# Optimization experiments

Measured on AMD Instinct MI355X. Metric: run time of the kernel, lower is better.

## Reference

```python
import jax, jax.numpy as jnp
import numpy as np
from jax import lax

DIM = 128
HEADS = 8
HEAD_DIM = DIM // HEADS
SR = 2
B, H, W = 2, 80, 80
SCALE = HEAD_DIM ** (-0.5)
BN_EPS = 1e-5


def _conv1x1(x, w, b):
    # x: (B,C,H,W), w: (O,C), b: (O,)
    return jnp.einsum('bchw,oc->bohw', x, w) + b[None, :, None, None]


def setup_inputs() -> dict:
    key = jax.random.key(0)
    ks = jax.random.split(key, 12)
    s = DIM ** -0.5
    x = jax.random.normal(ks[0], (B, DIM, H, W), dtype=jnp.float32)
    q_w = jax.random.normal(ks[1], (DIM, DIM), dtype=jnp.float32) * s
    q_b = jnp.zeros((DIM,), jnp.float32)
    k_w = jax.random.normal(ks[2], (DIM, DIM), dtype=jnp.float32) * s
    k_b = jnp.zeros((DIM,), jnp.float32)
    v_w = jax.random.normal(ks[3], (DIM, DIM), dtype=jnp.float32) * s
    v_b = jnp.zeros((DIM,), jnp.float32)
    sr_w = jax.random.normal(ks[4], (DIM, DIM, SR, SR), dtype=jnp.float32) * (s / SR)
    sr_b = jnp.zeros((DIM,), jnp.float32)
    bn_gamma = jnp.ones((DIM,), jnp.float32)
    bn_beta = jnp.zeros((DIM,), jnp.float32)
    bn_mean = jnp.zeros((DIM,), jnp.float32)
    bn_var = jnp.ones((DIM,), jnp.float32)
    proj_w = jax.random.normal(ks[5], (DIM, DIM), dtype=jnp.float32) * s
    proj_b = jnp.zeros((DIM,), jnp.float32)
    return dict(x=x, q_w=q_w, q_b=q_b, k_w=k_w, k_b=k_b, v_w=v_w, v_b=v_b,
                sr_w=sr_w, sr_b=sr_b, bn_gamma=bn_gamma, bn_beta=bn_beta,
                bn_mean=bn_mean, bn_var=bn_var, proj_w=proj_w, proj_b=proj_b)


def reference(x, q_w, q_b, k_w, k_b, v_w, v_b, sr_w, sr_b,
              bn_gamma, bn_beta, bn_mean, bn_var, proj_w, proj_b):
    b, c, h, w = x.shape
    n = h * w
    # q: (B,h,N,d)
    q = _conv1x1(x, q_w, q_b).reshape(b, HEADS, HEAD_DIM, n).transpose(0, 1, 3, 2)
    # spatial reduction: Conv2d(k=SR, s=SR) + BN(eval) + ReLU
    x_kv = lax.conv_general_dilated(x, sr_w, window_strides=(SR, SR),
                                    padding='VALID',
                                    dimension_numbers=('NCHW', 'OIHW', 'NCHW'))
    x_kv = x_kv + sr_b[None, :, None, None]
    inv = bn_gamma / jnp.sqrt(bn_var + BN_EPS)
    x_kv = x_kv * inv[None, :, None, None] + (bn_beta - bn_mean * inv)[None, :, None, None]
    x_kv = jax.nn.relu(x_kv)
    n_kv = x_kv.shape[2] * x_kv.shape[3]
    k = _conv1x1(x_kv, k_w, k_b).reshape(b, HEADS, HEAD_DIM, n_kv).transpose(0, 1, 3, 2)
    v = _conv1x1(x_kv, v_w, v_b).reshape(b, HEADS, HEAD_DIM, n_kv).transpose(0, 1, 3, 2)
    # explicit attention: (B,h,N,N_kv)
    attn = jnp.einsum('bhnd,bhmd->bhnm', q, k) * SCALE
    attn = jax.nn.softmax(attn, axis=-1)
    out = jnp.einsum('bhnm,bhmd->bhnd', attn, v)  # (B,h,N,d)
    # faithful to source layout: transpose(1,2) then reshape to (B,C,H,W)
    out = out.transpose(0, 2, 1, 3).reshape(b, c, h, w)
    out = _conv1x1(out, proj_w, proj_b)
    return out
```

## Files before the change

kernel.cpp:

```cpp
#include <hip/hip_runtime.h>
#include <hip/hip_bf16.h>
#include <cmath>

#define DIM 128
#define HEADS 8
#define HEAD_DIM 16
#define NBATCH 2
#define HH 80
#define WW 80
#define NQ 6400
#define NKV 1600
#define NC 50
#define BN_EPS 1e-5f
#define LOG2E 1.4426950408889634f

typedef __bf16 bf16_t;
typedef __attribute__((ext_vector_type(8))) __bf16 bf16x8;
typedef __attribute__((ext_vector_type(16))) float f32x16;

union BF8U { bf16x8 v; unsigned u[4]; };

__device__ inline unsigned packbf2(float a, float b) {
  union { __hip_bfloat162 v; unsigned u; } r;
  r.v = __float22bfloat162_rn(make_float2(a, b));
  return r.u;
}

__device__ inline unsigned short f2bf(float v) {
  unsigned u = __float_as_uint(v);
  return (unsigned short)((u + 0x7FFFu + ((u >> 16) & 1u)) >> 16);
}

__global__ __launch_bounds__(256) void prep_all(
    const float* __restrict__ x,
    const float* __restrict__ qw, const float* __restrict__ kw,
    const float* __restrict__ vw, const float* __restrict__ pw,
    const float* __restrict__ srw,
    unsigned short* __restrict__ Xb,
    unsigned short* __restrict__ Wb,
    unsigned short* __restrict__ X4b,
    unsigned short* __restrict__ Vp)
{
  __shared__ float tile[32][33];
  int t = threadIdx.x;
  int bx = blockIdx.x;
  if (bx < 1600) {
    int tx = t & 31, ty = t >> 5;
    int b = bx / 800;
    int rem = bx % 800;
    int c0 = (rem / 200) * 32, s0 = (rem % 200) * 32;
#pragma unroll
    for (int r = 0; r < 32; r += 8)
      tile[ty + r][tx] = x[((size_t)b * DIM + c0 + ty + r) * NQ + s0 + tx];
    __syncthreads();
#pragma unroll
    for (int r = 0; r < 32; r += 8)
      Xb[((size_t)b * NQ + s0 + ty + r) * DIM + c0 + tx] = f2bf(tile[tx][ty + r]);
    return;
  }
  int e = (bx - 1600) * 256 + t;
  if (e < 131072) {
    const float* src; int idx;
    if (e < 16384)      { src = qw;  idx = e; }
    else if (e < 32768) { src = kw;  idx = e - 16384; }
    else if (e < 49152) { src = vw;  idx = e - 32768; }
    else if (e < 65536) { src = pw;  idx = e - 49152; }
    else                { src = srw; idx = e - 65536; }
    Wb[e] = f2bf(src[idx]);
  }
  if (e < NBATCH * HEADS * NC * 32) {
    int cid = e >> 5;
    int pos = e & 31;
    size_t addr = (size_t)cid * 1024 + 256 + ((pos & 16) ? 512 : 0) + (pos & 15);
    Vp[addr] = 0x3F80;
  }
  int c4 = e & 511;
  int r = e >> 9;
  int b = r / 1600, m = r % 1600;
  int c = c4 >> 2, ky = (c4 >> 1) & 1, kx = c4 & 1;
  int i = m / 40, j = m % 40;
  X4b[e] = f2bf(x[((size_t)b * DIM + c) * NQ + (2 * i + ky) * WW + 2 * j + kx]);
}

__global__ __launch_bounds__(256) void mgemm_qsr(
    const bf16_t* __restrict__ Xb, const bf16_t* __restrict__ X4b,
    const bf16_t* __restrict__ Wb,
    const float* __restrict__ q_b, const float* __restrict__ sr_b,
    unsigned short* __restrict__ Qb, unsigned short* __restrict__ xkvb,
    float sl,
    const float* __restrict__ bng, const float* __restrict__ bnb,
    const float* __restrict__ bnm, const float* __restrict__ bnv)
{
  int t = threadIdx.x;
  int ln = t & 31, hf = (t >> 5) & 1, wid = t >> 6;
  int b = blockIdx.y;
  bool isq = blockIdx.x < 200;
  int s0 = isq ? blockIdx.x * 32 : (blockIdx.x - 200) * 32;
  int S  = isq ? NQ : NKV;
  int C  = isq ? 128 : 512;
  const bf16_t* X = isq ? Xb : X4b;
  const bf16_t* W = isq ? Wb : (Wb + 65536);
  int o = wid * 32 + ln;

  const bf16_t* arow = &X[((size_t)b * S + s0 + ln) * C + hf * 8];
  const bf16_t* brow = &W[(size_t)o * C + hf * 8];
  f32x16 acc = {};
#pragma unroll 8
  for (int c0 = 0; c0 < C; c0 += 16) {
    bf16x8 af = *(const bf16x8*)&arow[c0];
    bf16x8 bf = *(const bf16x8*)&brow[c0];
    acc = __builtin_amdgcn_mfma_f32_32x32x16_bf16(af, bf, acc, 0, 0, 0);
  }

  float bv, a1, b2;
  bool relu;
  if (isq) { bv = q_b[o]; a1 = sl; b2 = 0.f; relu = false; }
  else {
    bv = sr_b[o];
    float inv = bng[o] / sqrtf(bnv[o] + BN_EPS);
    a1 = inv; b2 = bnb[o] - bnm[o] * inv; relu = true;
  }
  unsigned short* ob = isq ? Qb : xkvb;
#pragma unroll
  for (int g = 0; g < 4; ++g)
#pragma unroll
    for (int j = 0; j < 4; ++j) {
      float v = (acc[4 * g + j] + bv) * a1 + b2;
      if (relu) v = fmaxf(v, 0.f);
      int s = s0 + 8 * g + 4 * hf + j;
      ob[((size_t)b * S + s) * DIM + o] = f2bf(v);
    }
}

__global__ __launch_bounds__(256) void mgemm_kv(
    const bf16_t* __restrict__ xkvb, const bf16_t* __restrict__ Wb,
    const float* __restrict__ k_b, const float* __restrict__ v_b,
    unsigned short* __restrict__ Kp, unsigned short* __restrict__ Vp)
{
  int t = threadIdx.x;
  int ln = t & 31, hf = (t >> 5) & 1, wid = t >> 6;
  int b = blockIdx.y;
  int isv = blockIdx.z;
  int s0 = blockIdx.x * 32;
  const bf16_t* W = Wb + (isv ? 32768 : 16384);
  int o = wid * 32 + ln;

  const bf16_t* arow = &xkvb[((size_t)b * NKV + s0 + ln) * DIM + hf * 8];
  const bf16_t* brow = &W[(size_t)o * DIM + hf * 8];
  f32x16 acc = {};
#pragma unroll
  for (int c0 = 0; c0 < 128; c0 += 16) {
    bf16x8 af = *(const bf16x8*)&arow[c0];
    bf16x8 bf = *(const bf16x8*)&brow[c0];
    acc = __builtin_amdgcn_mfma_f32_32x32x16_bf16(af, bf, acc, 0, 0, 0);
  }

  int hloc = o >> 4, d = o & 15;
  if (isv) {
    float bv = v_b[o];
    size_t CB = (((size_t)b * HEADS + hloc) * NC + (s0 >> 5)) * 1024;
    uint4 w0, w1;
    w0.x = packbf2(acc[0] + bv, acc[1] + bv);
    w0.y = packbf2(acc[2] + bv, acc[3] + bv);
    w0.z = packbf2(acc[4] + bv, acc[5] + bv);
    w0.w = packbf2(acc[6] + bv, acc[7] + bv);
    w1.x = packbf2(acc[8] + bv, acc[9] + bv);
    w1.y = packbf2(acc[10] + bv, acc[11] + bv);
    w1.z = packbf2(acc[12] + bv, acc[13] + bv);
    w1.w = packbf2(acc[14] + bv, acc[15] + bv);
    *(uint4*)&Vp[CB + d * 16 + hf * 8] = w0;
    *(uint4*)&Vp[CB + 512 + d * 16 + hf * 8] = w1;
  } else {
    float bv = k_b[o];
    size_t CB = (((size_t)b * HEADS + hloc) * NC + (s0 >> 5)) * 512;
#pragma unroll
    for (int g = 0; g < 4; ++g)
#pragma unroll
      for (int j = 0; j < 4; ++j) {
        int sl2 = 8 * g + 4 * hf + j;
        Kp[CB + sl2 * 16 + d] = f2bf(acc[4 * g + j] + bv);
      }
  }
}

__global__ __launch_bounds__(256) void attn_split(const bf16_t* __restrict__ Qb,
                                                  const bf16_t* __restrict__ Kp,
                                                  const bf16_t* __restrict__ Vp,
                                                  unsigned short* __restrict__ Pb,
                                                  float* __restrict__ Lsum)
{
  const int t = threadIdx.x;
  const int ln = t & 31, hf = (t >> 5) & 1, wid = t >> 6;
  const int h = blockIdx.y;
  const int b = blockIdx.z & 1, half = blockIdx.z >> 1;
  const int q0 = blockIdx.x * 128 + wid * 32;

  bf16x8 qf = *(const bf16x8*)&Qb[((size_t)b * NQ + q0 + ln) * 128 + h * 16 + hf * 8];
  const int bh = b * HEADS + h;
  const bf16_t* kc = &Kp[((size_t)bh * NC + half * 25) * 512 + ln * 16 + hf * 8];
  const bf16_t* vc = &Vp[((size_t)bh * NC + half * 25) * 1024 + ln * 16 + hf * 8];

  f32x16 acc = {};
  const f32x16 zero = {};

  bf16x8 kf = *(const bf16x8*)kc;
  bf16x8 va = *(const bf16x8*)vc;
  bf16x8 vb = *(const bf16x8*)(vc + 512);

  for (int c = 0; c < 25; ++c) {
    int cn = (c < 24) ? c + 1 : c;
    bf16x8 kf2 = *(const bf16x8*)(kc + cn * 512);
    bf16x8 va2 = *(const bf16x8*)(vc + cn * 1024);
    bf16x8 vb2 = *(const bf16x8*)(vc + cn * 1024 + 512);

    f32x16 S = __builtin_amdgcn_mfma_f32_32x32x16_bf16(kf, qf, zero, 0, 0, 0);

    BF8U f0, f1;
#pragma unroll
    for (int i = 0; i < 4; ++i) {
      f0.u[i] = packbf2(__builtin_amdgcn_exp2f(S[2 * i]),
                        __builtin_amdgcn_exp2f(S[2 * i + 1]));
      f1.u[i] = packbf2(__builtin_amdgcn_exp2f(S[8 + 2 * i]),
                        __builtin_amdgcn_exp2f(S[9 + 2 * i]));
    }

    acc = __builtin_amdgcn_mfma_f32_32x32x16_bf16(va, f0.v, acc, 0, 0, 0);
    acc = __builtin_amdgcn_mfma_f32_32x32x16_bf16(vb, f1.v, acc, 0, 0, 0);
    kf = kf2; va = va2; vb = vb2;
  }

  unsigned short* prow =
      &Pb[(((size_t)(half * 2 + b)) * NQ + q0 + ln) * 128 + h * 16 + 4 * hf];
  uint2 w0, w1;
  w0.x = packbf2(acc[0], acc[1]); w0.y = packbf2(acc[2], acc[3]);
  w1.x = packbf2(acc[4], acc[5]); w1.y = packbf2(acc[6], acc[7]);
  *(uint2*)&prow[0] = w0;
  *(uint2*)&prow[8] = w1;
  if (!hf)
    Lsum[(((size_t)(half * 2 + b)) * HEADS + h) * NQ + q0 + ln] = acc[8];
}

__global__ __launch_bounds__(256) void proj_comb(const unsigned short* __restrict__ Pb,
                                                 const float* __restrict__ Lsum,
                                                 const bf16_t* __restrict__ Wb,
                                                 const float* __restrict__ bias,
                                                 float* __restrict__ Out)
{
  __shared__ unsigned short As[32][136];
  int t = threadIdx.x;
  int b = blockIdx.y;
  int s0 = blockIdx.x * 32;

  {
    int tx = t & 31, cg = t >> 5;
#pragma unroll
    for (int it = 0; it < 16; ++it) {
      int c = cg * 16 + it;
      int f = c * NQ + s0 + tx;
      int n = f >> 7, hh = (f >> 4) & 7;
      float p0 = __uint_as_float((unsigned)Pb[(size_t)b * 819200 + f] << 16);
      float p1 = __uint_as_float((unsigned)Pb[(size_t)(2 + b) * 819200 + f] << 16);
      float L = Lsum[((size_t)b * HEADS + hh) * NQ + n] +
                Lsum[((size_t)(2 + b) * HEADS + hh) * NQ + n];
      As[tx][c] = f2bf((p0 + p1) / L);
    }
  }
  __syncthreads();

  int ln = t & 31, hf = (t >> 5) & 1, wid = t >> 6;
  int o = wid * 32 + ln;
  const bf16_t* brow = &Wb[49152 + (size_t)o * DIM + hf * 8];
  const unsigned short* arow = &As[ln][hf * 8];
  f32x16 acc = {};
#pragma unroll
  for (int c0 = 0; c0 < 128; c0 += 16) {
    bf16x8 af = *(const bf16x8*)&arow[c0];
    bf16x8 bf = *(const bf16x8*)&brow[c0];
    acc = __builtin_amdgcn_mfma_f32_32x32x16_bf16(af, bf, acc, 0, 0, 0);
  }
  float bv = bias[o];
  float* obase = &Out[((size_t)b * DIM + o) * NQ + s0 + 4 * hf];
#pragma unroll
  for (int g = 0; g < 4; ++g) {
    float4 r;
    r.x = acc[4 * g + 0] + bv; r.y = acc[4 * g + 1] + bv;
    r.z = acc[4 * g + 2] + bv; r.w = acc[4 * g + 3] + bv;
    *(float4*)&obase[8 * g] = r;
  }
}

extern "C" void kernel_launch(void* const* d_in, const int* in_sizes, int n_in,
                              void* d_out, int out_size, void* d_ws, size_t ws_size,
                              hipStream_t stream)
{
  const float* x    = (const float*)d_in[0];
  const float* q_w  = (const float*)d_in[1];
  const float* q_b  = (const float*)d_in[2];
  const float* k_w  = (const float*)d_in[3];
  const float* k_b  = (const float*)d_in[4];
  const float* v_w  = (const float*)d_in[5];
  const float* v_b  = (const float*)d_in[6];
  const float* sr_w = (const float*)d_in[7];
  const float* sr_b = (const float*)d_in[8];
  const float* bng  = (const float*)d_in[9];
  const float* bnb  = (const float*)d_in[10];
  const float* bnm  = (const float*)d_in[11];
  const float* bnv  = (const float*)d_in[12];
  const float* p_w  = (const float*)d_in[13];
  const float* p_b  = (const float*)d_in[14];
  float* out = (float*)d_out;

  float* ws = (float*)d_ws;
  bf16_t* Xb   = (bf16_t*)(ws);
  bf16_t* X4b  = (bf16_t*)(ws + 819200);
  bf16_t* xkvb = (bf16_t*)(ws + 1638400);
  bf16_t* Pb   = (bf16_t*)(ws);
  bf16_t* Qb   = (bf16_t*)(ws + 1843200);
  bf16_t* Kp   = (bf16_t*)(ws + 2662400);
  bf16_t* Vp   = (bf16_t*)(ws + 2867200);
  float*  Lsum = ws + 3276800;
  bf16_t* Wb   = (bf16_t*)(ws + 3481600);

  const float sl = 0.25f * LOG2E;

  prep_all<<<dim3(8000), dim3(256), 0, stream>>>(
      x, q_w, k_w, v_w, p_w, sr_w,
      (unsigned short*)Xb, (unsigned short*)Wb,
      (unsigned short*)X4b, (unsigned short*)Vp);

  mgemm_qsr<<<dim3(250, NBATCH), dim3(256), 0, stream>>>(
      Xb, X4b, Wb, q_b, sr_b, (unsigned short*)Qb, (unsigned short*)xkvb,
      sl, bng, bnb, bnm, bnv);

  mgemm_kv<<<dim3(NKV / 32, NBATCH, 2), dim3(256), 0, stream>>>(
      xkvb, Wb, k_b, v_b, (unsigned short*)Kp, (unsigned short*)Vp);

  attn_split<<<dim3(NQ / 128, HEADS, 4), dim3(256), 0, stream>>>(
      Qb, Kp, Vp, (unsigned short*)Pb, Lsum);

  proj_comb<<<dim3(200, NBATCH), dim3(256), 0, stream>>>(
      (const unsigned short*)Pb, Lsum, Wb, p_b, out);
}
```

Before: 161.5 us.

## Fuse input prep into GEMMs, generalize attention KV split count

Removes the separate prep kernel. The Q and spatial-reduction GEMMs now read fp32 x directly, gathering the strided or 2x2 patch elements and converting to bf16 in registers. Weights are converted from fp32 on the fly in every GEMM, and the V ones-column padding moves into the V GEMM. Attention gets a configurable KV split count (4 when the workspace allows) with a simpler non-prefetching loop and launch bounds for higher occupancy, and the projection kernel reduces across all splits. This trades one launch and its intermediate buffers for uncoalesced strided global reads in the Q/SR GEMM and more partial-sum traffic.

```diff
diff --git a/kernel.cpp b/kernel.cpp
--- a/kernel.cpp
+++ b/kernel.cpp
@@ -4,10 +4,7 @@
 
 #define DIM 128
 #define HEADS 8
-#define HEAD_DIM 16
 #define NBATCH 2
-#define HH 80
-#define WW 80
 #define NQ 6400
 #define NKV 1600
 #define NC 50
@@ -31,110 +28,89 @@
   return (unsigned short)((u + 0x7FFFu + ((u >> 16) & 1u)) >> 16);
 }
 
-__global__ __launch_bounds__(256) void prep_all(
+__device__ inline bf16x8 ldw8(const float* __restrict__ p) {
+  float4 w0 = *(const float4*)p;
+  float4 w1 = *(const float4*)(p + 4);
+  BF8U r;
+  r.u[0] = packbf2(w0.x, w0.y);
+  r.u[1] = packbf2(w0.z, w0.w);
+  r.u[2] = packbf2(w1.x, w1.y);
+  r.u[3] = packbf2(w1.z, w1.w);
+  return r.v;
+}
+
+__global__ __launch_bounds__(256) void mgemm_qsr(
     const float* __restrict__ x,
-    const float* __restrict__ qw, const float* __restrict__ kw,
-    const float* __restrict__ vw, const float* __restrict__ pw,
-    const float* __restrict__ srw,
-    unsigned short* __restrict__ Xb,
-    unsigned short* __restrict__ Wb,
-    unsigned short* __restrict__ X4b,
-    unsigned short* __restrict__ Vp)
-{
-  __shared__ float tile[32][33];
-  int t = threadIdx.x;
-  int bx = blockIdx.x;
-  if (bx < 1600) {
-    int tx = t & 31, ty = t >> 5;
-    int b = bx / 800;
-    int rem = bx % 800;
-    int c0 = (rem / 200) * 32, s0 = (rem % 200) * 32;
-#pragma unroll
-    for (int r = 0; r < 32; r += 8)
-      tile[ty + r][tx] = x[((size_t)b * DIM + c0 + ty + r) * NQ + s0 + tx];
-    __syncthreads();
-#pragma unroll
-    for (int r = 0; r < 32; r += 8)
-      Xb[((size_t)b * NQ + s0 + ty + r) * DIM + c0 + tx] = f2bf(tile[tx][ty + r]);
-    return;
-  }
-  int e = (bx - 1600) * 256 + t;
-  if (e < 131072) {
-    const float* src; int idx;
-    if (e < 16384)      { src = qw;  idx = e; }
-    else if (e < 32768) { src = kw;  idx = e - 16384; }
-    else if (e < 49152) { src = vw;  idx = e - 32768; }
-    else if (e < 65536) { src = pw;  idx = e - 49152; }
-    else                { src = srw; idx = e - 65536; }
-    Wb[e] = f2bf(src[idx]);
-  }
-  if (e < NBATCH * HEADS * NC * 32) {
-    int cid = e >> 5;
-    int pos = e & 31;
-    size_t addr = (size_t)cid * 1024 + 256 + ((pos & 16) ? 512 : 0) + (pos & 15);
-    Vp[addr] = 0x3F80;
-  }
-  int c4 = e & 511;
-  int r = e >> 9;
-  int b = r / 1600, m = r % 1600;
-  int c = c4 >> 2, ky = (c4 >> 1) & 1, kx = c4 & 1;
-  int i = m / 40, j = m % 40;
-  X4b[e] = f2bf(x[((size_t)b * DIM + c) * NQ + (2 * i + ky) * WW + 2 * j + kx]);
-}
-
-__global__ __launch_bounds__(256) void mgemm_qsr(
-    const bf16_t* __restrict__ Xb, const bf16_t* __restrict__ X4b,
-    const bf16_t* __restrict__ Wb,
-    const float* __restrict__ q_b, const float* __restrict__ sr_b,
+    const float* __restrict__ q_w, const float* __restrict__ q_b,
+    const float* __restrict__ sr_w, const float* __restrict__ sr_b,
+    const float* __restrict__ bng, const float* __restrict__ bnb,
+    const float* __restrict__ bnm, const float* __restrict__ bnv,
     unsigned short* __restrict__ Qb, unsigned short* __restrict__ xkvb,
-    float sl,
-    const float* __restrict__ bng, const float* __restrict__ bnb,
-    const float* __restrict__ bnm, const float* __restrict__ bnv)
+    float sl)
 {
   int t = threadIdx.x;
   int ln = t & 31, hf = (t >> 5) & 1, wid = t >> 6;
   int b = blockIdx.y;
-  bool isq = blockIdx.x < 200;
-  int s0 = isq ? blockIdx.x * 32 : (blockIdx.x - 200) * 32;
-  int S  = isq ? NQ : NKV;
-  int C  = isq ? 128 : 512;
-  const bf16_t* X = isq ? Xb : X4b;
-  const bf16_t* W = isq ? Wb : (Wb + 65536);
   int o = wid * 32 + ln;
-
-  const bf16_t* arow = &X[((size_t)b * S + s0 + ln) * C + hf * 8];
-  const bf16_t* brow = &W[(size_t)o * C + hf * 8];
   f32x16 acc = {};
-#pragma unroll 8
-  for (int c0 = 0; c0 < C; c0 += 16) {
-    bf16x8 af = *(const bf16x8*)&arow[c0];
-    bf16x8 bf = *(const bf16x8*)&brow[c0];
-    acc = __builtin_amdgcn_mfma_f32_32x32x16_bf16(af, bf, acc, 0, 0, 0);
-  }
-
-  float bv, a1, b2;
-  bool relu;
-  if (isq) { bv = q_b[o]; a1 = sl; b2 = 0.f; relu = false; }
-  else {
-    bv = sr_b[o];
+
+  if (blockIdx.x < 200) {
+    int s0 = blockIdx.x * 32;
+    const float* ab = x + (size_t)b * DIM * NQ + s0 + ln;
+    const float* brow = q_w + (size_t)o * 128 + hf * 8;
+#pragma unroll
+    for (int c0 = 0; c0 < 128; c0 += 16) {
+      BF8U af;
+#pragma unroll
+      for (int jj = 0; jj < 4; ++jj)
+        af.u[jj] = packbf2(ab[(size_t)(c0 + hf * 8 + 2 * jj) * NQ],
+                           ab[(size_t)(c0 + hf * 8 + 2 * jj + 1) * NQ]);
+      acc = __builtin_amdgcn_mfma_f32_32x32x16_bf16(af.v, ldw8(&brow[c0]), acc, 0, 0, 0);
+    }
+    float bv = q_b[o];
+#pragma unroll
+    for (int g = 0; g < 4; ++g)
+#pragma unroll
+      for (int j = 0; j < 4; ++j) {
+        int s = s0 + 8 * g + 4 * hf + j;
+        Qb[((size_t)b * NQ + s) * DIM + o] = f2bf((acc[4 * g + j] + bv) * sl);
+      }
+  } else {
+    int s0 = (blockIdx.x - 200) * 32;
+    int m = s0 + ln;
+    int i = m / 40, jp = m % 40;
+    const float* ab = x + (size_t)b * DIM * NQ + i * 160 + 2 * jp;
+    const float* brow = sr_w + (size_t)o * 512 + hf * 8;
+#pragma unroll 4
+    for (int c0 = 0; c0 < 512; c0 += 16) {
+      BF8U af;
+#pragma unroll
+      for (int jj = 0; jj < 4; ++jj) {
+        int ca = c0 + hf * 8 + 2 * jj, cb = ca + 1;
+        float va_ = ab[(size_t)(ca >> 2) * NQ + ((ca >> 1) & 1) * 80 + (ca & 1)];
+        float vb_ = ab[(size_t)(cb >> 2) * NQ + ((cb >> 1) & 1) * 80 + (cb & 1)];
+        af.u[jj] = packbf2(va_, vb_);
+      }
+      acc = __builtin_amdgcn_mfma_f32_32x32x16_bf16(af.v, ldw8(&brow[c0]), acc, 0, 0, 0);
+    }
+    float bv = sr_b[o];
     float inv = bng[o] / sqrtf(bnv[o] + BN_EPS);
-    a1 = inv; b2 = bnb[o] - bnm[o] * inv; relu = true;
-  }
-  unsigned short* ob = isq ? Qb : xkvb;
-#pragma unroll
-  for (int g = 0; g < 4; ++g)
-#pragma unroll
-    for (int j = 0; j < 4; ++j) {
-      float v = (acc[4 * g + j] + bv) * a1 + b2;
-      if (relu) v = fmaxf(v, 0.f);
-      int s = s0 + 8 * g + 4 * hf + j;
-      ob[((size_t)b * S + s) * DIM + o] = f2bf(v);
-    }
+    float b2 = bnb[o] - bnm[o] * inv;
+#pragma unroll
+    for (int g = 0; g < 4; ++g)
+#pragma unroll
+      for (int j = 0; j < 4; ++j) {
+        int s = s0 + 8 * g + 4 * hf + j;
+        float v = fmaxf((acc[4 * g + j] + bv) * inv + b2, 0.f);
+        xkvb[((size_t)b * NKV + s) * DIM + o] = f2bf(v);
+      }
+  }
 }
 
 __global__ __launch_bounds__(256) void mgemm_kv(
-    const bf16_t* __restrict__ xkvb, const bf16_t* __restrict__ Wb,
-    const float* __restrict__ k_b, const float* __restrict__ v_b,
+    const bf16_t* __restrict__ xkvb,
+    const float* __restrict__ k_w, const float* __restrict__ k_b,
+    const float* __restrict__ v_w, const float* __restrict__ v_b,
     unsigned short* __restrict__ Kp, unsigned short* __restrict__ Vp)
 {
   int t = threadIdx.x;
@@ -142,17 +118,16 @@
   int b = blockIdx.y;
   int isv = blockIdx.z;
   int s0 = blockIdx.x * 32;
-  const bf16_t* W = Wb + (isv ? 32768 : 16384);
+  const float* W = isv ? v_w : k_w;
   int o = wid * 32 + ln;
 
   const bf16_t* arow = &xkvb[((size_t)b * NKV + s0 + ln) * DIM + hf * 8];
-  const bf16_t* brow = &W[(size_t)o * DIM + hf * 8];
+  const float* brow = W + (size_t)o * DIM + hf * 8;
   f32x16 acc = {};
 #pragma unroll
   for (int c0 = 0; c0 < 128; c0 += 16) {
     bf16x8 af = *(const bf16x8*)&arow[c0];
-    bf16x8 bf = *(const bf16x8*)&brow[c0];
-    acc = __builtin_amdgcn_mfma_f32_32x32x16_bf16(af, bf, acc, 0, 0, 0);
+    acc = __builtin_amdgcn_mfma_f32_32x32x16_bf16(af, ldw8(&brow[c0]), acc, 0, 0, 0);
   }
 
   int hloc = o >> 4, d = o & 15;
@@ -170,6 +145,11 @@
     w1.w = packbf2(acc[14] + bv, acc[15] + bv);
     *(uint4*)&Vp[CB + d * 16 + hf * 8] = w0;
     *(uint4*)&Vp[CB + 512 + d * 16 + hf * 8] = w1;
+    {
+      int h2 = t >> 5, pos = t & 31;
+      size_t CB2 = (((size_t)b * HEADS + h2) * NC + (s0 >> 5)) * 1024;
+      Vp[CB2 + 256 + ((pos & 16) ? 512 : 0) + (pos & 15)] = 0x3F80;
+    }
   } else {
     float bv = k_b[o];
     size_t CB = (((size_t)b * HEADS + hloc) * NC + (s0 >> 5)) * 512;
@@ -183,35 +163,33 @@
   }
 }
 
-__global__ __launch_bounds__(256) void attn_split(const bf16_t* __restrict__ Qb,
-                                                  const bf16_t* __restrict__ Kp,
-                                                  const bf16_t* __restrict__ Vp,
-                                                  unsigned short* __restrict__ Pb,
-                                                  float* __restrict__ Lsum)
+__global__ __launch_bounds__(256, 8) void attn_split(
+    const bf16_t* __restrict__ Qb, const bf16_t* __restrict__ Kp,
+    const bf16_t* __restrict__ Vp, unsigned short* __restrict__ Pb,
+    float* __restrict__ Lsum, int nsplit)
 {
   const int t = threadIdx.x;
   const int ln = t & 31, hf = (t >> 5) & 1, wid = t >> 6;
   const int h = blockIdx.y;
-  const int b = blockIdx.z & 1, half = blockIdx.z >> 1;
+  const int b = blockIdx.z & 1, quarter = blockIdx.z >> 1;
   const int q0 = blockIdx.x * 128 + wid * 32;
-
-  bf16x8 qf = *(const bf16x8*)&Qb[((size_t)b * NQ + q0 + ln) * 128 + h * 16 + hf * 8];
+  const int base = NC / nsplit, rem = NC % nsplit;
+  const int kcnt = base + (quarter < rem ? 1 : 0);
+  const int kstart = quarter * base + (quarter < rem ? quarter : rem);
+  const int slice = quarter * 2 + b;
+
+  bf16x8 qf = *(const bf16x8*)&Qb[((size_t)b * NQ + q0 + ln) * DIM + h * 16 + hf * 8];
   const int bh = b * HEADS + h;
-  const bf16_t* kc = &Kp[((size_t)bh * NC + half * 25) * 512 + ln * 16 + hf * 8];
-  const bf16_t* vc = &Vp[((size_t)bh * NC + half * 25) * 1024 + ln * 16 + hf * 8];
+  const bf16_t* kc = &Kp[((size_t)bh * NC + kstart) * 512 + ln * 16 + hf * 8];
+  const bf16_t* vc = &Vp[((size_t)bh * NC + kstart) * 1024 + ln * 16 + hf * 8];
 
   f32x16 acc = {};
   const f32x16 zero = {};
 
-  bf16x8 kf = *(const bf16x8*)kc;
-  bf16x8 va = *(const bf16x8*)vc;
-  bf16x8 vb = *(const bf16x8*)(vc + 512);
-
-  for (int c = 0; c < 25; ++c) {
-    int cn = (c < 24) ? c + 1 : c;
-    bf16x8 kf2 = *(const bf16x8*)(kc + cn * 512);
-    bf16x8 va2 = *(const bf16x8*)(vc + cn * 1024);
-    bf16x8 vb2 = *(const bf16x8*)(vc + cn * 1024 + 512);
+  for (int c = 0; c < kcnt; ++c) {
+    bf16x8 kf = *(const bf16x8*)kc;
+    bf16x8 va = *(const bf16x8*)vc;
+    bf16x8 vb = *(const bf16x8*)(vc + 512);
 
     f32x16 S = __builtin_amdgcn_mfma_f32_32x32x16_bf16(kf, qf, zero, 0, 0, 0);
 
@@ -226,25 +204,24 @@
 
     acc = __builtin_amdgcn_mfma_f32_32x32x16_bf16(va, f0.v, acc, 0, 0, 0);
     acc = __builtin_amdgcn_mfma_f32_32x32x16_bf16(vb, f1.v, acc, 0, 0, 0);
-    kf = kf2; va = va2; vb = vb2;
+    kc += 512; vc += 1024;
   }
 
   unsigned short* prow =
-      &Pb[(((size_t)(half * 2 + b)) * NQ + q0 + ln) * 128 + h * 16 + 4 * hf];
+      &Pb[(size_t)slice * (NQ * DIM) + (size_t)(q0 + ln) * DIM + h * 16 + 4 * hf];
   uint2 w0, w1;
   w0.x = packbf2(acc[0], acc[1]); w0.y = packbf2(acc[2], acc[3]);
   w1.x = packbf2(acc[4], acc[5]); w1.y = packbf2(acc[6], acc[7]);
   *(uint2*)&prow[0] = w0;
   *(uint2*)&prow[8] = w1;
   if (!hf)
-    Lsum[(((size_t)(half * 2 + b)) * HEADS + h) * NQ + q0 + ln] = acc[8];
-}
-
-__global__ __launch_bounds__(256) void proj_comb(const unsigned short* __restrict__ Pb,
-                                                 const float* __restrict__ Lsum,
-                                                 const bf16_t* __restrict__ Wb,
-                                                 const float* __restrict__ bias,
-                                                 float* __restrict__ Out)
+    Lsum[(size_t)slice * (HEADS * NQ) + (size_t)h * NQ + q0 + ln] = acc[8];
+}
+
+__global__ __launch_bounds__(256) void proj_comb(
+    const unsigned short* __restrict__ Pb, const float* __restrict__ Lsum,
+    const float* __restrict__ p_w, const float* __restrict__ p_b,
+    float* __restrict__ Out, int nsplit)
 {
   __shared__ unsigned short As[32][136];
   int t = threadIdx.x;
@@ -258,27 +235,28 @@
       int c = cg * 16 + it;
       int f = c * NQ + s0 + tx;
       int n = f >> 7, hh = (f >> 4) & 7;
-      float p0 = __uint_as_float((unsigned)Pb[(size_t)b * 819200 + f] << 16);
-      float p1 = __uint_as_float((unsigned)Pb[(size_t)(2 + b) * 819200 + f] << 16);
-      float L = Lsum[((size_t)b * HEADS + hh) * NQ + n] +
-                Lsum[((size_t)(2 + b) * HEADS + hh) * NQ + n];
-      As[tx][c] = f2bf((p0 + p1) / L);
+      float ps = 0.f, L = 0.f;
+      for (int qq = 0; qq < nsplit; ++qq) {
+        int sl2 = qq * 2 + b;
+        ps += __uint_as_float((unsigned)Pb[(size_t)sl2 * (NQ * DIM) + f] << 16);
+        L += Lsum[(size_t)sl2 * (HEADS * NQ) + (size_t)hh * NQ + n];
+      }
+      As[tx][c] = f2bf(ps / L);
     }
   }
   __syncthreads();
 
   int ln = t & 31, hf = (t >> 5) & 1, wid = t >> 6;
   int o = wid * 32 + ln;
-  const bf16_t* brow = &Wb[49152 + (size_t)o * DIM + hf * 8];
+  const float* brow = p_w + (size_t)o * DIM + hf * 8;
   const unsigned short* arow = &As[ln][hf * 8];
   f32x16 acc = {};
 #pragma unroll
   for (int c0 = 0; c0 < 128; c0 += 16) {
     bf16x8 af = *(const bf16x8*)&arow[c0];
-    bf16x8 bf = *(const bf16x8*)&brow[c0];
-    acc = __builtin_amdgcn_mfma_f32_32x32x16_bf16(af, bf, acc, 0, 0, 0);
-  }
-  float bv = bias[o];
+    acc = __builtin_amdgcn_mfma_f32_32x32x16_bf16(af, ldw8(&brow[c0]), acc, 0, 0, 0);
+  }
+  float bv = p_b[o];
   float* obase = &Out[((size_t)b * DIM + o) * NQ + s0 + 4 * hf];
 #pragma unroll
   for (int g = 0; g < 4; ++g) {
@@ -310,34 +288,29 @@
   const float* p_b  = (const float*)d_in[14];
   float* out = (float*)d_out;
 
+  const int nsplit = (ws_size >= (size_t)5120000 * 4) ? 4 : 2;
+
   float* ws = (float*)d_ws;
-  bf16_t* Xb   = (bf16_t*)(ws);
-  bf16_t* X4b  = (bf16_t*)(ws + 819200);
-  bf16_t* xkvb = (bf16_t*)(ws + 1638400);
-  bf16_t* Pb   = (bf16_t*)(ws);
-  bf16_t* Qb   = (bf16_t*)(ws + 1843200);
-  bf16_t* Kp   = (bf16_t*)(ws + 2662400);
-  bf16_t* Vp   = (bf16_t*)(ws + 2867200);
-  float*  Lsum = ws + 3276800;
-  bf16_t* Wb   = (bf16_t*)(ws + 3481600);
+  bf16_t* Pb   = (bf16_t*)ws;
+  bf16_t* xkvb = (bf16_t*)ws;
+  size_t off = (size_t)nsplit * 819200;
+  bf16_t* Qb = (bf16_t*)(ws + off);   off += 819200;
+  bf16_t* Kp = (bf16_t*)(ws + off);   off += 204800;
+  bf16_t* Vp = (bf16_t*)(ws + off);   off += 409600;
+  float* Lsum = ws + off;
 
   const float sl = 0.25f * LOG2E;
 
-  prep_all<<<dim3(8000), dim3(256), 0, stream>>>(
-      x, q_w, k_w, v_w, p_w, sr_w,
-      (unsigned short*)Xb, (unsigned short*)Wb,
-      (unsigned short*)X4b, (unsigned short*)Vp);
-
   mgemm_qsr<<<dim3(250, NBATCH), dim3(256), 0, stream>>>(
-      Xb, X4b, Wb, q_b, sr_b, (unsigned short*)Qb, (unsigned short*)xkvb,
-      sl, bng, bnb, bnm, bnv);
+      x, q_w, q_b, sr_w, sr_b, bng, bnb, bnm, bnv,
+      (unsigned short*)Qb, (unsigned short*)xkvb, sl);
 
   mgemm_kv<<<dim3(NKV / 32, NBATCH, 2), dim3(256), 0, stream>>>(
-      xkvb, Wb, k_b, v_b, (unsigned short*)Kp, (unsigned short*)Vp);
-
-  attn_split<<<dim3(NQ / 128, HEADS, 4), dim3(256), 0, stream>>>(
-      Qb, Kp, Vp, (unsigned short*)Pb, Lsum);
+      xkvb, k_w, k_b, v_w, v_b, (unsigned short*)Kp, (unsigned short*)Vp);
+
+  attn_split<<<dim3(NQ / 128, HEADS, 2 * nsplit), dim3(256), 0, stream>>>(
+      Qb, Kp, Vp, (unsigned short*)Pb, Lsum, nsplit);
 
   proj_comb<<<dim3(200, NBATCH), dim3(256), 0, stream>>>(
-      (const unsigned short*)Pb, Lsum, Wb, p_b, out);
-}
+      (const unsigned short*)Pb, Lsum, p_w, p_b, out, nsplit);
+}
```

After: 168.6 us. 1.04x slower.

## Generalize attention KV split to configurable count, use four splits when workspace allows

Applied to the files above, without the earlier changes.

The attention kernel now splits the KV chunks across a runtime-chosen number of partitions (four if the workspace is large enough, else two), raising the block count from 800 to 1600 for more parallelism on the GPU. The projection kernel sums the partial outputs and softmax denominators over all splits. The Pb buffer moves to its own workspace region instead of aliasing Xb, and the software prefetch of the next K/V chunk is removed in favor of plain in-loop loads with an occupancy hint. The cost is more partial-result traffic and extra reduction work in the combine step.

```diff
diff --git a/kernel.cpp b/kernel.cpp
--- a/kernel.cpp
+++ b/kernel.cpp
@@ -4,10 +4,7 @@
 
 #define DIM 128
 #define HEADS 8
-#define HEAD_DIM 16
 #define NBATCH 2
-#define HH 80
-#define WW 80
 #define NQ 6400
 #define NKV 1600
 #define NC 50
@@ -79,7 +76,7 @@
   int b = r / 1600, m = r % 1600;
   int c = c4 >> 2, ky = (c4 >> 1) & 1, kx = c4 & 1;
   int i = m / 40, j = m % 40;
-  X4b[e] = f2bf(x[((size_t)b * DIM + c) * NQ + (2 * i + ky) * WW + 2 * j + kx]);
+  X4b[e] = f2bf(x[((size_t)b * DIM + c) * NQ + (2 * i + ky) * 80 + 2 * j + kx]);
 }
 
 __global__ __launch_bounds__(256) void mgemm_qsr(
@@ -183,35 +180,33 @@
   }
 }
 
-__global__ __launch_bounds__(256) void attn_split(const bf16_t* __restrict__ Qb,
-                                                  const bf16_t* __restrict__ Kp,
-                                                  const bf16_t* __restrict__ Vp,
-                                                  unsigned short* __restrict__ Pb,
-                                                  float* __restrict__ Lsum)
+__global__ __launch_bounds__(256, 8) void attn_split(
+    const bf16_t* __restrict__ Qb, const bf16_t* __restrict__ Kp,
+    const bf16_t* __restrict__ Vp, unsigned short* __restrict__ Pb,
+    float* __restrict__ Lsum, int nsplit)
 {
   const int t = threadIdx.x;
   const int ln = t & 31, hf = (t >> 5) & 1, wid = t >> 6;
   const int h = blockIdx.y;
-  const int b = blockIdx.z & 1, half = blockIdx.z >> 1;
+  const int b = blockIdx.z & 1, quarter = blockIdx.z >> 1;
   const int q0 = blockIdx.x * 128 + wid * 32;
-
-  bf16x8 qf = *(const bf16x8*)&Qb[((size_t)b * NQ + q0 + ln) * 128 + h * 16 + hf * 8];
+  const int base = NC / nsplit, rem = NC % nsplit;
+  const int kcnt = base + (quarter < rem ? 1 : 0);
+  const int kstart = quarter * base + (quarter < rem ? quarter : rem);
+  const int slice = quarter * 2 + b;
+
+  bf16x8 qf = *(const bf16x8*)&Qb[((size_t)b * NQ + q0 + ln) * DIM + h * 16 + hf * 8];
   const int bh = b * HEADS + h;
-  const bf16_t* kc = &Kp[((size_t)bh * NC + half * 25) * 512 + ln * 16 + hf * 8];
-  const bf16_t* vc = &Vp[((size_t)bh * NC + half * 25) * 1024 + ln * 16 + hf * 8];
+  const bf16_t* kc = &Kp[((size_t)bh * NC + kstart) * 512 + ln * 16 + hf * 8];
+  const bf16_t* vc = &Vp[((size_t)bh * NC + kstart) * 1024 + ln * 16 + hf * 8];
 
   f32x16 acc = {};
   const f32x16 zero = {};
 
-  bf16x8 kf = *(const bf16x8*)kc;
-  bf16x8 va = *(const bf16x8*)vc;
-  bf16x8 vb = *(const bf16x8*)(vc + 512);
-
-  for (int c = 0; c < 25; ++c) {
-    int cn = (c < 24) ? c + 1 : c;
-    bf16x8 kf2 = *(const bf16x8*)(kc + cn * 512);
-    bf16x8 va2 = *(const bf16x8*)(vc + cn * 1024);
-    bf16x8 vb2 = *(const bf16x8*)(vc + cn * 1024 + 512);
+  for (int c = 0; c < kcnt; ++c) {
+    bf16x8 kf = *(const bf16x8*)kc;
+    bf16x8 va = *(const bf16x8*)vc;
+    bf16x8 vb = *(const bf16x8*)(vc + 512);
 
     f32x16 S = __builtin_amdgcn_mfma_f32_32x32x16_bf16(kf, qf, zero, 0, 0, 0);
 
@@ -226,27 +221,26 @@
 
     acc = __builtin_amdgcn_mfma_f32_32x32x16_bf16(va, f0.v, acc, 0, 0, 0);
     acc = __builtin_amdgcn_mfma_f32_32x32x16_bf16(vb, f1.v, acc, 0, 0, 0);
-    kf = kf2; va = va2; vb = vb2;
+    kc += 512; vc += 1024;
   }
 
   unsigned short* prow =
-      &Pb[(((size_t)(half * 2 + b)) * NQ + q0 + ln) * 128 + h * 16 + 4 * hf];
+      &Pb[(size_t)slice * (NQ * DIM) + (size_t)(q0 + ln) * DIM + h * 16 + 4 * hf];
   uint2 w0, w1;
   w0.x = packbf2(acc[0], acc[1]); w0.y = packbf2(acc[2], acc[3]);
   w1.x = packbf2(acc[4], acc[5]); w1.y = packbf2(acc[6], acc[7]);
   *(uint2*)&prow[0] = w0;
   *(uint2*)&prow[8] = w1;
   if (!hf)
-    Lsum[(((size_t)(half * 2 + b)) * HEADS + h) * NQ + q0 + ln] = acc[8];
-}
-
-__global__ __launch_bounds__(256) void proj_comb(const unsigned short* __restrict__ Pb,
-                                                 const float* __restrict__ Lsum,
-                                                 const bf16_t* __restrict__ Wb,
-                                                 const float* __restrict__ bias,
-                                                 float* __restrict__ Out)
-{
-  __shared__ unsigned short As[32][136];
+    Lsum[(size_t)slice * (HEADS * NQ) + (size_t)h * NQ + q0 + ln] = acc[8];
+}
+
+__global__ __launch_bounds__(256) void proj_comb(
+    const unsigned short* __restrict__ Pb, const float* __restrict__ Lsum,
+    const bf16_t* __restrict__ Wb, const float* __restrict__ p_b,
+    float* __restrict__ Out, int nsplit)
+{
+  __shared__ __align__(16) unsigned short As[32][136];
   int t = threadIdx.x;
   int b = blockIdx.y;
   int s0 = blockIdx.x * 32;
@@ -258,11 +252,13 @@
       int c = cg * 16 + it;
       int f = c * NQ + s0 + tx;
       int n = f >> 7, hh = (f >> 4) & 7;
-      float p0 = __uint_as_float((unsigned)Pb[(size_t)b * 819200 + f] << 16);
-      float p1 = __uint_as_float((unsigned)Pb[(size_t)(2 + b) * 819200 + f] << 16);
-      float L = Lsum[((size_t)b * HEADS + hh) * NQ + n] +
-                Lsum[((size_t)(2 + b) * HEADS + hh) * NQ + n];
-      As[tx][c] = f2bf((p0 + p1) / L);
+      float ps = 0.f, L = 0.f;
+      for (int qq = 0; qq < nsplit; ++qq) {
+        int sl2 = qq * 2 + b;
+        ps += __uint_as_float((unsigned)Pb[(size_t)sl2 * (NQ * DIM) + f] << 16);
+        L += Lsum[(size_t)sl2 * (HEADS * NQ) + (size_t)hh * NQ + n];
+      }
+      As[tx][c] = f2bf(ps / L);
     }
   }
   __syncthreads();
@@ -278,7 +274,7 @@
     bf16x8 bf = *(const bf16x8*)&brow[c0];
     acc = __builtin_amdgcn_mfma_f32_32x32x16_bf16(af, bf, acc, 0, 0, 0);
   }
-  float bv = bias[o];
+  float bv = p_b[o];
   float* obase = &Out[((size_t)b * DIM + o) * NQ + s0 + 4 * hf];
 #pragma unroll
   for (int g = 0; g < 4; ++g) {
@@ -314,12 +310,14 @@
   bf16_t* Xb   = (bf16_t*)(ws);
   bf16_t* X4b  = (bf16_t*)(ws + 819200);
   bf16_t* xkvb = (bf16_t*)(ws + 1638400);
-  bf16_t* Pb   = (bf16_t*)(ws);
   bf16_t* Qb   = (bf16_t*)(ws + 1843200);
   bf16_t* Kp   = (bf16_t*)(ws + 2662400);
   bf16_t* Vp   = (bf16_t*)(ws + 2867200);
   float*  Lsum = ws + 3276800;
-  bf16_t* Wb   = (bf16_t*)(ws + 3481600);
+  bf16_t* Wb   = (bf16_t*)(ws + 3686400);
+  bf16_t* Pb   = (bf16_t*)(ws + 3751936);
+
+  const int nsplit = (ws_size >= (size_t)7028736 * 4) ? 4 : 2;
 
   const float sl = 0.25f * LOG2E;
 
@@ -335,9 +333,9 @@
   mgemm_kv<<<dim3(NKV / 32, NBATCH, 2), dim3(256), 0, stream>>>(
       xkvb, Wb, k_b, v_b, (unsigned short*)Kp, (unsigned short*)Vp);
 
-  attn_split<<<dim3(NQ / 128, HEADS, 4), dim3(256), 0, stream>>>(
-      Qb, Kp, Vp, (unsigned short*)Pb, Lsum);
+  attn_split<<<dim3(NQ / 128, HEADS, 2 * nsplit), dim3(256), 0, stream>>>(
+      Qb, Kp, Vp, (unsigned short*)Pb, Lsum, nsplit);
 
   proj_comb<<<dim3(200, NBATCH), dim3(256), 0, stream>>>(
-      (const unsigned short*)Pb, Lsum, Wb, p_b, out);
-}
+      (const unsigned short*)Pb, Lsum, Wb, p_b, out, nsplit);
+}
```

Measured after the change: 166.8 us. 1.03x slower.

## Fuse spatial-reduction conv with K/V projection in one GEMM kernel

Applied to the files above, without the earlier changes.

Merges the Q/SR GEMM and K/V GEMM kernels into one launch. The SR-conv blocks keep the BN+ReLU output tile in shared memory and immediately compute K and V from it, removing the xkvb global round trip and one kernel launch. Q blocks run in the same grid. The workspace layout is reshuffled, with Pb moved to its own region. The trade-off is that the 50 KV blocks per batch do more serial work, which may lengthen the tail of the grid.

```diff
diff --git a/kernel.cpp b/kernel.cpp
--- a/kernel.cpp
+++ b/kernel.cpp
@@ -4,10 +4,7 @@
 
 #define DIM 128
 #define HEADS 8
-#define HEAD_DIM 16
 #define NBATCH 2
-#define HH 80
-#define WW 80
 #define NQ 6400
 #define NKV 1600
 #define NC 50
@@ -79,106 +76,106 @@
   int b = r / 1600, m = r % 1600;
   int c = c4 >> 2, ky = (c4 >> 1) & 1, kx = c4 & 1;
   int i = m / 40, j = m % 40;
-  X4b[e] = f2bf(x[((size_t)b * DIM + c) * NQ + (2 * i + ky) * WW + 2 * j + kx]);
-}
-
-__global__ __launch_bounds__(256) void mgemm_qsr(
+  X4b[e] = f2bf(x[((size_t)b * DIM + c) * NQ + (2 * i + ky) * 80 + 2 * j + kx]);
+}
+
+__global__ __launch_bounds__(256) void mgemm_qsrkv(
     const bf16_t* __restrict__ Xb, const bf16_t* __restrict__ X4b,
     const bf16_t* __restrict__ Wb,
     const float* __restrict__ q_b, const float* __restrict__ sr_b,
-    unsigned short* __restrict__ Qb, unsigned short* __restrict__ xkvb,
-    float sl,
+    const float* __restrict__ k_b, const float* __restrict__ v_b,
     const float* __restrict__ bng, const float* __restrict__ bnb,
-    const float* __restrict__ bnm, const float* __restrict__ bnv)
-{
+    const float* __restrict__ bnm, const float* __restrict__ bnv,
+    unsigned short* __restrict__ Qb,
+    unsigned short* __restrict__ Kp, unsigned short* __restrict__ Vp,
+    float sl)
+{
+  __shared__ __align__(16) unsigned short xs[32][136];
   int t = threadIdx.x;
   int ln = t & 31, hf = (t >> 5) & 1, wid = t >> 6;
   int b = blockIdx.y;
-  bool isq = blockIdx.x < 200;
-  int s0 = isq ? blockIdx.x * 32 : (blockIdx.x - 200) * 32;
-  int S  = isq ? NQ : NKV;
-  int C  = isq ? 128 : 512;
-  const bf16_t* X = isq ? Xb : X4b;
-  const bf16_t* W = isq ? Wb : (Wb + 65536);
   int o = wid * 32 + ln;
 
-  const bf16_t* arow = &X[((size_t)b * S + s0 + ln) * C + hf * 8];
-  const bf16_t* brow = &W[(size_t)o * C + hf * 8];
-  f32x16 acc = {};
+  if (blockIdx.x < 50) {
+    int s0 = blockIdx.x * 32;
+    const bf16_t* arow = &X4b[((size_t)b * NKV + s0 + ln) * 512 + hf * 8];
+    const bf16_t* brow = &Wb[65536 + (size_t)o * 512 + hf * 8];
+    f32x16 acc = {};
 #pragma unroll 8
-  for (int c0 = 0; c0 < C; c0 += 16) {
-    bf16x8 af = *(const bf16x8*)&arow[c0];
-    bf16x8 bf = *(const bf16x8*)&brow[c0];
-    acc = __builtin_amdgcn_mfma_f32_32x32x16_bf16(af, bf, acc, 0, 0, 0);
-  }
-
-  float bv, a1, b2;
-  bool relu;
-  if (isq) { bv = q_b[o]; a1 = sl; b2 = 0.f; relu = false; }
-  else {
-    bv = sr_b[o];
+    for (int c0 = 0; c0 < 512; c0 += 16) {
+      bf16x8 af = *(const bf16x8*)&arow[c0];
+      bf16x8 bf = *(const bf16x8*)&brow[c0];
+      acc = __builtin_amdgcn_mfma_f32_32x32x16_bf16(af, bf, acc, 0, 0, 0);
+    }
+    float bv = sr_b[o];
     float inv = bng[o] / sqrtf(bnv[o] + BN_EPS);
-    a1 = inv; b2 = bnb[o] - bnm[o] * inv; relu = true;
-  }
-  unsigned short* ob = isq ? Qb : xkvb;
-#pragma unroll
-  for (int g = 0; g < 4; ++g)
-#pragma unroll
-    for (int j = 0; j < 4; ++j) {
-      float v = (acc[4 * g + j] + bv) * a1 + b2;
-      if (relu) v = fmaxf(v, 0.f);
-      int s = s0 + 8 * g + 4 * hf + j;
-      ob[((size_t)b * S + s) * DIM + o] = f2bf(v);
-    }
-}
-
-__global__ __launch_bounds__(256) void mgemm_kv(
-    const bf16_t* __restrict__ xkvb, const bf16_t* __restrict__ Wb,
-    const float* __restrict__ k_b, const float* __restrict__ v_b,
-    unsigned short* __restrict__ Kp, unsigned short* __restrict__ Vp)
-{
-  int t = threadIdx.x;
-  int ln = t & 31, hf = (t >> 5) & 1, wid = t >> 6;
-  int b = blockIdx.y;
-  int isv = blockIdx.z;
-  int s0 = blockIdx.x * 32;
-  const bf16_t* W = Wb + (isv ? 32768 : 16384);
-  int o = wid * 32 + ln;
-
-  const bf16_t* arow = &xkvb[((size_t)b * NKV + s0 + ln) * DIM + hf * 8];
-  const bf16_t* brow = &W[(size_t)o * DIM + hf * 8];
-  f32x16 acc = {};
-#pragma unroll
-  for (int c0 = 0; c0 < 128; c0 += 16) {
-    bf16x8 af = *(const bf16x8*)&arow[c0];
-    bf16x8 bf = *(const bf16x8*)&brow[c0];
-    acc = __builtin_amdgcn_mfma_f32_32x32x16_bf16(af, bf, acc, 0, 0, 0);
-  }
-
-  int hloc = o >> 4, d = o & 15;
-  if (isv) {
-    float bv = v_b[o];
-    size_t CB = (((size_t)b * HEADS + hloc) * NC + (s0 >> 5)) * 1024;
-    uint4 w0, w1;
-    w0.x = packbf2(acc[0] + bv, acc[1] + bv);
-    w0.y = packbf2(acc[2] + bv, acc[3] + bv);
-    w0.z = packbf2(acc[4] + bv, acc[5] + bv);
-    w0.w = packbf2(acc[6] + bv, acc[7] + bv);
-    w1.x = packbf2(acc[8] + bv, acc[9] + bv);
-    w1.y = packbf2(acc[10] + bv, acc[11] + bv);
-    w1.z = packbf2(acc[12] + bv, acc[13] + bv);
-    w1.w = packbf2(acc[14] + bv, acc[15] + bv);
-    *(uint4*)&Vp[CB + d * 16 + hf * 8] = w0;
-    *(uint4*)&Vp[CB + 512 + d * 16 + hf * 8] = w1;
+    float b2 = bnb[o] - bnm[o] * inv;
+#pragma unroll
+    for (int g = 0; g < 4; ++g)
+#pragma unroll
+      for (int j = 0; j < 4; ++j) {
+        int s = 8 * g + 4 * hf + j;
+        xs[s][o] = f2bf(fmaxf((acc[4 * g + j] + bv) * inv + b2, 0.f));
+      }
+    __syncthreads();
+
+    const unsigned short* ar2 = &xs[ln][hf * 8];
+    const bf16_t* kbrow = &Wb[16384 + (size_t)o * DIM + hf * 8];
+    const bf16_t* vbrow = &Wb[32768 + (size_t)o * DIM + hf * 8];
+    f32x16 ka = {}, va = {};
+#pragma unroll
+    for (int c0 = 0; c0 < 128; c0 += 16) {
+      bf16x8 af = *(const bf16x8*)&ar2[c0];
+      bf16x8 kb = *(const bf16x8*)&kbrow[c0];
+      bf16x8 vb = *(const bf16x8*)&vbrow[c0];
+      ka = __builtin_amdgcn_mfma_f32_32x32x16_bf16(af, kb, ka, 0, 0, 0);
+      va = __builtin_amdgcn_mfma_f32_32x32x16_bf16(af, vb, va, 0, 0, 0);
+    }
+    int hloc = o >> 4, d = o & 15;
+    {
+      float kb2 = k_b[o];
+      size_t CB = (((size_t)b * HEADS + hloc) * NC + (s0 >> 5)) * 512;
+#pragma unroll
+      for (int g = 0; g < 4; ++g)
+#pragma unroll
+        for (int j = 0; j < 4; ++j) {
+          int sl2 = 8 * g + 4 * hf + j;
+          Kp[CB + sl2 * 16 + d] = f2bf(ka[4 * g + j] + kb2);
+        }
+    }
+    {
+      float vb2 = v_b[o];
+      size_t CB = (((size_t)b * HEADS + hloc) * NC + (s0 >> 5)) * 1024;
+      uint4 w0, w1;
+      w0.x = packbf2(va[0] + vb2, va[1] + vb2);
+      w0.y = packbf2(va[2] + vb2, va[3] + vb2);
+      w0.z = packbf2(va[4] + vb2, va[5] + vb2);
+      w0.w = packbf2(va[6] + vb2, va[7] + vb2);
+      w1.x = packbf2(va[8] + vb2, va[9] + vb2);
+      w1.y = packbf2(va[10] + vb2, va[11] + vb2);
+      w1.z = packbf2(va[12] + vb2, va[13] + vb2);
+      w1.w = packbf2(va[14] + vb2, va[15] + vb2);
+      *(uint4*)&Vp[CB + d * 16 + hf * 8] = w0;
+      *(uint4*)&Vp[CB + 512 + d * 16 + hf * 8] = w1;
+    }
   } else {
-    float bv = k_b[o];
-    size_t CB = (((size_t)b * HEADS + hloc) * NC + (s0 >> 5)) * 512;
+    int s0 = (blockIdx.x - 50) * 32;
+    const bf16_t* arow = &Xb[((size_t)b * NQ + s0 + ln) * DIM + hf * 8];
+    const bf16_t* brow = &Wb[(size_t)o * DIM + hf * 8];
+    f32x16 acc = {};
+#pragma unroll
+    for (int c0 = 0; c0 < 128; c0 += 16) {
+      bf16x8 af = *(const bf16x8*)&arow[c0];
+      bf16x8 bf = *(const bf16x8*)&brow[c0];
+      acc = __builtin_amdgcn_mfma_f32_32x32x16_bf16(af, bf, acc, 0, 0, 0);
+    }
+    float bv = q_b[o];
 #pragma unroll
     for (int g = 0; g < 4; ++g)
 #pragma unroll
       for (int j = 0; j < 4; ++j) {
-        int sl2 = 8 * g + 4 * hf + j;
-        Kp[CB + sl2 * 16 + d] = f2bf(acc[4 * g + j] + bv);
+        int s = s0 + 8 * g + 4 * hf + j;
+        Qb[((size_t)b * NQ + s) * DIM + o] = f2bf((acc[4 * g + j] + bv) * sl);
       }
   }
 }
@@ -195,7 +192,7 @@
   const int b = blockIdx.z & 1, half = blockIdx.z >> 1;
   const int q0 = blockIdx.x * 128 + wid * 32;
 
-  bf16x8 qf = *(const bf16x8*)&Qb[((size_t)b * NQ + q0 + ln) * 128 + h * 16 + hf * 8];
+  bf16x8 qf = *(const bf16x8*)&Qb[((size_t)b * NQ + q0 + ln) * DIM + h * 16 + hf * 8];
   const int bh = b * HEADS + h;
   const bf16_t* kc = &Kp[((size_t)bh * NC + half * 25) * 512 + ln * 16 + hf * 8];
   const bf16_t* vc = &Vp[((size_t)bh * NC + half * 25) * 1024 + ln * 16 + hf * 8];
@@ -230,23 +227,22 @@
   }
 
   unsigned short* prow =
-      &Pb[(((size_t)(half * 2 + b)) * NQ + q0 + ln) * 128 + h * 16 + 4 * hf];
+      &Pb[(size_t)(half * 2 + b) * (NQ * DIM) + (size_t)(q0 + ln) * DIM + h * 16 + 4 * hf];
   uint2 w0, w1;
   w0.x = packbf2(acc[0], acc[1]); w0.y = packbf2(acc[2], acc[3]);
   w1.x = packbf2(acc[4], acc[5]); w1.y = packbf2(acc[6], acc[7]);
   *(uint2*)&prow[0] = w0;
   *(uint2*)&prow[8] = w1;
   if (!hf)
-    Lsum[(((size_t)(half * 2 + b)) * HEADS + h) * NQ + q0 + ln] = acc[8];
-}
-
-__global__ __launch_bounds__(256) void proj_comb(const unsigned short* __restrict__ Pb,
-                                                 const float* __restrict__ Lsum,
-                                                 const bf16_t* __restrict__ Wb,
-                                                 const float* __restrict__ bias,
-                                                 float* __restrict__ Out)
-{
-  __shared__ unsigned short As[32][136];
+    Lsum[(size_t)(half * 2 + b) * (HEADS * NQ) + (size_t)h * NQ + q0 + ln] = acc[8];
+}
+
+__global__ __launch_bounds__(256) void proj_comb(
+    const unsigned short* __restrict__ Pb, const float* __restrict__ Lsum,
+    const bf16_t* __restrict__ Wb, const float* __restrict__ p_b,
+    float* __restrict__ Out)
+{
+  __shared__ __align__(16) unsigned short As[32][136];
   int t = threadIdx.x;
   int b = blockIdx.y;
   int s0 = blockIdx.x * 32;
@@ -258,10 +254,10 @@
       int c = cg * 16 + it;
       int f = c * NQ + s0 + tx;
       int n = f >> 7, hh = (f >> 4) & 7;
-      float p0 = __uint_as_float((unsigned)Pb[(size_t)b * 819200 + f] << 16);
-      float p1 = __uint_as_float((unsigned)Pb[(size_t)(2 + b) * 819200 + f] << 16);
-      float L = Lsum[((size_t)b * HEADS + hh) * NQ + n] +
-                Lsum[((size_t)(2 + b) * HEADS + hh) * NQ + n];
+      float p0 = __uint_as_float((unsigned)Pb[(size_t)b * (NQ * DIM) + f] << 16);
+      float p1 = __uint_as_float((unsigned)Pb[(size_t)(2 + b) * (NQ * DIM) + f] << 16);
+      float L = Lsum[(size_t)b * (HEADS * NQ) + (size_t)hh * NQ + n] +
+                Lsum[(size_t)(2 + b) * (HEADS * NQ) + (size_t)hh * NQ + n];
       As[tx][c] = f2bf((p0 + p1) / L);
     }
   }
@@ -278,7 +274,7 @@
     bf16x8 bf = *(const bf16x8*)&brow[c0];
     acc = __builtin_amdgcn_mfma_f32_32x32x16_bf16(af, bf, acc, 0, 0, 0);
   }
-  float bv = bias[o];
+  float bv = p_b[o];
   float* obase = &Out[((size_t)b * DIM + o) * NQ + s0 + 4 * hf];
 #pragma unroll
   for (int g = 0; g < 4; ++g) {
@@ -313,13 +309,12 @@
   float* ws = (float*)d_ws;
   bf16_t* Xb   = (bf16_t*)(ws);
   bf16_t* X4b  = (bf16_t*)(ws + 819200);
-  bf16_t* xkvb = (bf16_t*)(ws + 1638400);
-  bf16_t* Pb   = (bf16_t*)(ws);
-  bf16_t* Qb   = (bf16_t*)(ws + 1843200);
-  bf16_t* Kp   = (bf16_t*)(ws + 2662400);
-  bf16_t* Vp   = (bf16_t*)(ws + 2867200);
-  float*  Lsum = ws + 3276800;
-  bf16_t* Wb   = (bf16_t*)(ws + 3481600);
+  bf16_t* Qb   = (bf16_t*)(ws + 1638400);
+  bf16_t* Kp   = (bf16_t*)(ws + 2457600);
+  bf16_t* Vp   = (bf16_t*)(ws + 2662400);
+  float*  Lsum = ws + 3072000;
+  bf16_t* Wb   = (bf16_t*)(ws + 3276800);
+  bf16_t* Pb   = (bf16_t*)(ws + 3342336);
 
   const float sl = 0.25f * LOG2E;
 
@@ -328,12 +323,9 @@
       (unsigned short*)Xb, (unsigned short*)Wb,
       (unsigned short*)X4b, (unsigned short*)Vp);
 
-  mgemm_qsr<<<dim3(250, NBATCH), dim3(256), 0, stream>>>(
-      Xb, X4b, Wb, q_b, sr_b, (unsigned short*)Qb, (unsigned short*)xkvb,
-      sl, bng, bnb, bnm, bnv);
-
-  mgemm_kv<<<dim3(NKV / 32, NBATCH, 2), dim3(256), 0, stream>>>(
-      xkvb, Wb, k_b, v_b, (unsigned short*)Kp, (unsigned short*)Vp);
+  mgemm_qsrkv<<<dim3(250, NBATCH), dim3(256), 0, stream>>>(
+      Xb, X4b, Wb, q_b, sr_b, k_b, v_b, bng, bnb, bnm, bnv,
+      (unsigned short*)Qb, (unsigned short*)Kp, (unsigned short*)Vp, sl);
 
   attn_split<<<dim3(NQ / 128, HEADS, 4), dim3(256), 0, stream>>>(
       Qb, Kp, Vp, (unsigned short*)Pb, Lsum);
```

Result: no change. 162.3 us (+0.5%).
